# Optimization experiments

Measured on AMD Instinct MI355X. Metric: run time of the kernel, lower is better.

Reference implementation:

```python
import jax, jax.numpy as jnp
import numpy as np
import math

D_EMB = 1024
N_HEADS = 16
D_HEAD = D_EMB // N_HEADS
D_FF = 4 * D_EMB
BATCH = 2
SEQ = 2048
EPS = 1e-6


def setup_inputs() -> dict:
    key = jax.random.key(0)
    ks = jax.random.split(key, 12)
    s = 0.02
    return {
        "x": jax.random.normal(ks[0], (BATCH, SEQ, D_EMB), jnp.float32),
        "wq": jax.random.normal(ks[1], (D_EMB, D_EMB), jnp.float32) * s,
        "wk": jax.random.normal(ks[2], (D_EMB, D_EMB), jnp.float32) * s,
        "wv": jax.random.normal(ks[3], (D_EMB, D_EMB), jnp.float32) * s,
        "wo": jax.random.normal(ks[4], (D_EMB, D_EMB), jnp.float32) * s,
        "bo": jnp.zeros((D_EMB,), jnp.float32),
        "w1": jax.random.normal(ks[5], (D_FF, D_EMB), jnp.float32) * s,
        "b1": jnp.zeros((D_FF,), jnp.float32),
        "w2": jax.random.normal(ks[6], (D_EMB, D_FF), jnp.float32) * s,
        "b2": jnp.zeros((D_EMB,), jnp.float32),
        "ln1_s": jnp.ones((D_EMB,), jnp.float32),
        "ln1_b": jnp.zeros((D_EMB,), jnp.float32),
        "ln2_s": jnp.ones((D_EMB,), jnp.float32),
        "ln2_b": jnp.zeros((D_EMB,), jnp.float32),
    }


def _layernorm(x, scale, shift):
    mean = jnp.mean(x, axis=-1, keepdims=True)
    var = jnp.mean(jnp.square(x - mean), axis=-1, keepdims=True)  # unbiased=False
    return scale * (x - mean) / jnp.sqrt(var + EPS) + shift


def _gelu_tanh(x):
    c = math.sqrt(2.0 / math.pi)
    return 0.5 * x * (1.0 + jnp.tanh(c * (x + 0.044715 * x * x * x)))


def _attention(x, wq, wk, wv, wo, bo):
    B, S, _ = x.shape
    q = (x @ wq.T).reshape(B, S, N_HEADS, D_HEAD).transpose(0, 2, 1, 3)
    k = (x @ wk.T).reshape(B, S, N_HEADS, D_HEAD).transpose(0, 2, 1, 3)
    v = (x @ wv.T).reshape(B, S, N_HEADS, D_HEAD).transpose(0, 2, 1, 3)
    scores = jnp.einsum("bhqd,bhkd->bhqk", q, k)
    causal = jnp.triu(jnp.ones((S, S), bool), k=1)
    scores = jnp.where(causal, -jnp.inf, scores)
    weights = jax.nn.softmax(scores / math.sqrt(D_HEAD), axis=-1)
    ctx = jnp.einsum("bhqk,bhkd->bhqd", weights, v)
    ctx = ctx.transpose(0, 2, 1, 3).reshape(B, S, D_EMB)
    return ctx @ wo.T + bo


def reference(x, wq, wk, wv, wo, bo, w1, b1, w2, b2, ln1_s, ln1_b, ln2_s, ln2_b):
    # pre-norm attention block (dropout in eval mode = identity)
    h = x + _attention(_layernorm(x, ln1_s, ln1_b), wq, wk, wv, wo, bo)
    # pre-norm MLP with tanh-approx GeLU
    y = _layernorm(h, ln2_s, ln2_b)
    y = _gelu_tanh(y @ w1.T + b1) @ w2.T + b2
    return h + y
```

## Files before the change

kernel.cpp:

```cpp
#include <hip/hip_runtime.h>
#include <math.h>

typedef unsigned short u16;
typedef __attribute__((ext_vector_type(8))) __bf16 bf16x8v;
typedef __attribute__((ext_vector_type(8))) unsigned short ushort8v;
typedef __attribute__((ext_vector_type(4))) unsigned short ushort4v;
typedef __attribute__((ext_vector_type(4))) float f32x4v;

#define D_EMBD 1024
#define NHEADS 16
#define DHEAD  64
#define DFF    4096
#define BATCHN 2
#define SEQL   2048
#define TOK    (BATCHN*SEQL)

#define EPI_BF16_GELU    2
#define EPI_BF16_QKV     3
#define EPI_BF16_PART    5

__device__ __forceinline__ float bf2f(u16 s) {
  return __builtin_bit_cast(float, (unsigned)s << 16);
}
__device__ __forceinline__ u16 f2bf(float f) {
  unsigned u = __builtin_bit_cast(unsigned, f);
  unsigned r = u + 0x7fffu + ((u >> 16) & 1u);
  return (u16)(r >> 16);
}
__device__ __forceinline__ u16 f2bf_trunc(float f) {
  return (u16)(__builtin_bit_cast(unsigned, f) >> 16);
}

#define GLOAD16(gp, lp)                                                        \
  __builtin_amdgcn_global_load_lds(                                            \
      (__attribute__((address_space(1))) void*)(void*)(gp),                    \
      (__attribute__((address_space(3))) void*)(void*)(lp), 16, 0, 0)

__global__ __launch_bounds__(256) void cvt_all_kernel(const float* __restrict__ wq,
                                                      const float* __restrict__ wk,
                                                      const float* __restrict__ wv,
                                                      const float* __restrict__ wo,
                                                      const float* __restrict__ w1,
                                                      const float* __restrict__ w2,
                                                      u16* __restrict__ wcat,
                                                      u16* __restrict__ wob,
                                                      u16* __restrict__ w1b,
                                                      u16* __restrict__ w2b) {
  int bid = blockIdx.x;
  const float* src;
  u16* dst;
  int loc;
  if (bid < 4096) {
    int seg = bid >> 10;
    loc = (bid & 1023) * 256 + threadIdx.x;
    src = (seg == 0) ? wq : (seg == 1) ? wk : (seg == 2) ? wv : wo;
    dst = (seg == 0) ? wcat : (seg == 1) ? wcat + 1048576
                            : (seg == 2) ? wcat + 2097152 : wob;
  } else if (bid < 8192) {
    loc = (bid - 4096) * 256 + threadIdx.x;
    src = w1; dst = w1b;
  } else {
    loc = (bid - 8192) * 256 + threadIdx.x;
    src = w2; dst = w2b;
  }
  float4 v = ((const float4*)src)[loc];
  ushort4 o;
  o.x = f2bf(v.x); o.y = f2bf(v.y); o.z = f2bf(v.z); o.w = f2bf(v.w);
  ((ushort4*)dst)[loc] = o;
}

__global__ __launch_bounds__(256) void ln_kernel(const float* __restrict__ x,
                                                 const float* __restrict__ sc,
                                                 const float* __restrict__ sh,
                                                 u16* __restrict__ out) {
  int row = blockIdx.x, tid = threadIdx.x;
  const float4* xr = (const float4*)(x + (size_t)row * D_EMBD);
  float4 v = xr[tid];
  float s  = (v.x + v.y) + (v.z + v.w);
  float s2 = (v.x * v.x + v.y * v.y) + (v.z * v.z + v.w * v.w);
#pragma unroll
  for (int off = 32; off; off >>= 1) {
    s  += __shfl_xor(s, off, 64);
    s2 += __shfl_xor(s2, off, 64);
  }
  __shared__ float rs[4], rs2[4];
  int wave = tid >> 6, lane = tid & 63;
  if (lane == 0) { rs[wave] = s; rs2[wave] = s2; }
  __syncthreads();
  s  = (rs[0] + rs[1]) + (rs[2] + rs[3]);
  s2 = (rs2[0] + rs2[1]) + (rs2[2] + rs2[3]);
  float mean = s * (1.f / 1024.f);
  float var  = s2 * (1.f / 1024.f) - mean * mean;
  float rstd = rsqrtf(var + 1e-6f);
  float4 scv = ((const float4*)sc)[tid];
  float4 shv = ((const float4*)sh)[tid];
  ushort4 o;
  o.x = f2bf((v.x - mean) * rstd * scv.x + shv.x);
  o.y = f2bf((v.y - mean) * rstd * scv.y + shv.y);
  o.z = f2bf((v.z - mean) * rstd * scv.z + shv.z);
  o.w = f2bf((v.w - mean) * rstd * scv.w + shv.w);
  ((ushort4*)(out + (size_t)row * D_EMBD))[tid] = o;
}

__global__ __launch_bounds__(256) void ln2f_kernel(const u16* __restrict__ parts,
                                                   const float* __restrict__ x,
                                                   const float* __restrict__ bo,
                                                   const float* __restrict__ sc,
                                                   const float* __restrict__ sh,
                                                   float* __restrict__ hbuf,
                                                   u16* __restrict__ ybuf) {
  int row = blockIdx.x, tid = threadIdx.x;
  size_t base4 = (size_t)row * 256 + tid;
  float4 v = ((const float4*)x)[base4];
  float4 bv = ((const float4*)bo)[tid];
  v.x += bv.x; v.y += bv.y; v.z += bv.z; v.w += bv.w;
#pragma unroll
  for (int p = 0; p < 4; ++p) {
    ushort4 u = ((const ushort4*)parts)[(size_t)p * 1048576 + base4];
    v.x += bf2f(u.x); v.y += bf2f(u.y); v.z += bf2f(u.z); v.w += bf2f(u.w);
  }
  ((float4*)hbuf)[base4] = v;
  float s  = (v.x + v.y) + (v.z + v.w);
  float s2 = (v.x * v.x + v.y * v.y) + (v.z * v.z + v.w * v.w);
#pragma unroll
  for (int off = 32; off; off >>= 1) {
    s  += __shfl_xor(s, off, 64);
    s2 += __shfl_xor(s2, off, 64);
  }
  __shared__ float rs[4], rs2[4];
  int wave = tid >> 6, lane = tid & 63;
  if (lane == 0) { rs[wave] = s; rs2[wave] = s2; }
  __syncthreads();
  s  = (rs[0] + rs[1]) + (rs[2] + rs[3]);
  s2 = (rs2[0] + rs2[1]) + (rs2[2] + rs2[3]);
  float mean = s * (1.f / 1024.f);
  float var  = s2 * (1.f / 1024.f) - mean * mean;
  float rstd = rsqrtf(var + 1e-6f);
  float4 scv = ((const float4*)sc)[tid];
  float4 shv = ((const float4*)sh)[tid];
  ushort4 o;
  o.x = f2bf((v.x - mean) * rstd * scv.x + shv.x);
  o.y = f2bf((v.y - mean) * rstd * scv.y + shv.y);
  o.z = f2bf((v.z - mean) * rstd * scv.z + shv.z);
  o.w = f2bf((v.w - mean) * rstd * scv.w + shv.w);
  ((ushort4*)ybuf)[base4] = o;
}

__global__ __launch_bounds__(256) void reduce_w2_kernel(const u16* __restrict__ parts,
                                                        const float* __restrict__ resid,
                                                        const float* __restrict__ bias,
                                                        float* __restrict__ out) {
  int i = blockIdx.x * 256 + threadIdx.x;
  float4 r = ((const float4*)resid)[i];
  float4 bi = ((const float4*)bias)[i & 255];
  float s0 = 0, s1 = 0, s2 = 0, s3 = 0;
#pragma unroll
  for (int p = 0; p < 4; ++p) {
    ushort4 u = ((const ushort4*)parts)[(size_t)p * 1048576 + i];
    s0 += bf2f(u.x); s1 += bf2f(u.y); s2 += bf2f(u.z); s3 += bf2f(u.w);
  }
  float4 o = {s0 + r.x + bi.x, s1 + r.y + bi.y, s2 + r.z + bi.z, s3 + r.w + bi.w};
  ((float4*)out)[i] = o;
}

#define GBAR  __builtin_amdgcn_s_barrier()
#define LGKM0 do { asm volatile("s_waitcnt lgkmcnt(0)" ::: "memory"); \
                   __builtin_amdgcn_sched_barrier(0); } while (0)

template <int EPI>
__global__ __launch_bounds__(512, 2) void gemm256(const u16* __restrict__ A,
                                                  const u16* __restrict__ W,
                                                  u16* __restrict__ Cb,
                                                  const float* __restrict__ bias,
                                                  int M, int N, int K) {
  __shared__ __align__(16) u16 sm[65536];
  const int tid = threadIdx.x;
  const int wave = tid >> 6, lane = tid & 63;
  const int lr = lane & 15, quad = lane >> 4;
  const int wm = wave >> 2, wn = wave & 3;
  const int gx = gridDim.x, gy = gridDim.y;
  const int nwg = gx * gy * gridDim.z;
  const int bid = blockIdx.x + gx * (blockIdx.y + gy * blockIdx.z);
  const int swz = (bid & 7) * (nwg >> 3) + (bid >> 3);
  const int bx = swz % gx;
  const int r1 = swz / gx;
  const int by = r1 % gy, bz = r1 / gy;
  const int m0 = by * 256, n0 = bx * 256;
  const int KC = K / gridDim.z;
  const int kbeg = bz * KC;
  const int NT = KC >> 6;
  const size_t poff = (size_t)bz * ((size_t)M * N);

  const int r8 = lane >> 3;
  const int sslot = (lane & 7) ^ r8;
  const int rb0 = wave * 2;
  const int sx = lr & 7;

  auto stA = [&](int bb, int h, int tk) {
#pragma unroll
    for (int s = 0; s < 2; ++s) {
      const u16* gp = A + (size_t)(m0 + h * 128 + (rb0 + s) * 8 + r8) * K +
                      (kbeg + tk * 64 + sslot * 8);
      GLOAD16(gp, (char*)sm + bb * 65536 + h * 16384 + (rb0 + s) * 1024);
    }
  };
  auto stB = [&](int bb, int h, int tk) {
#pragma unroll
    for (int s = 0; s < 2; ++s) {
      const u16* gp = W + (size_t)(n0 + h * 128 + (rb0 + s) * 8 + r8) * K +
                      (kbeg + tk * 64 + sslot * 8);
      GLOAD16(gp, (char*)sm + bb * 65536 + 32768 + h * 16384 + (rb0 + s) * 1024);
    }
  };
  auto ldA = [&](bf16x8v (&av)[4][2], int mh, int cur) {
#pragma unroll
    for (int j2 = 0; j2 < 4; ++j2) {
      int row = (2 * (mh * 4 + j2) + wm) * 16 + lr;
#pragma unroll
      for (int kk = 0; kk < 2; ++kk) {
        int slot = (kk * 4 + quad) ^ sx;
        av[j2][kk] = *(const bf16x8v*)(sm + cur * 32768 + row * 64 + slot * 8);
      }
    }
  };
  auto ldB = [&](bf16x8v (&bv)[2][2], int nh, int cur) {
#pragma unroll
    for (int i2 = 0; i2 < 2; ++i2) {
      int row = (wn + 4 * (nh * 2 + i2)) * 16 + lr;
#pragma unroll
      for (int kk = 0; kk < 2; ++kk) {
        int slot = (kk * 4 + quad) ^ sx;
        bv[i2][kk] = *(const bf16x8v*)(sm + cur * 32768 + 16384 + row * 64 + slot * 8);
      }
    }
  };

  f32x4v acc[8][4];
#pragma unroll
  for (int j = 0; j < 8; ++j)
#pragma unroll
    for (int i = 0; i < 4; ++i) {
      f32x4v z = {0.f, 0.f, 0.f, 0.f};
      acc[j][i] = z;
    }
  bf16x8v av[4][2], bv0[2][2], bv1[2][2];

  auto MMA = [&](int mh, int nh, bf16x8v (&a)[4][2], bf16x8v (&b)[2][2]) {
    GBAR;
    LGKM0;
    __builtin_amdgcn_s_setprio(1);
#pragma unroll
    for (int j2 = 0; j2 < 4; ++j2)
#pragma unroll
      for (int i2 = 0; i2 < 2; ++i2)
#pragma unroll
        for (int kk = 0; kk < 2; ++kk)
          acc[mh * 4 + j2][nh * 2 + i2] = __builtin_amdgcn_mfma_f32_16x16x32_bf16(
              a[j2][kk], b[i2][kk], acc[mh * 4 + j2][nh * 2 + i2], 0, 0, 0);
    __builtin_amdgcn_s_setprio(0);
    __builtin_amdgcn_sched_barrier(0);
    GBAR;
  };

  stA(0, 0, 0); stB(0, 0, 0); stA(0, 1, 0); stB(0, 1, 0);
  stA(1, 0, 1); stB(1, 1, 1);
  asm volatile("s_waitcnt vmcnt(4)" ::: "memory");
  GBAR;

  for (int t = 0; t < NT; ++t) {
    const int cur = t & 1, nb = cur ^ 1;
    const bool p1 = (t + 1 < NT), p2 = (t + 2 < NT);
    ldA(av, 0, cur); ldB(bv0, 0, cur);
    if (p1) stB(nb, 0, t + 1);
    MMA(0, 0, av, bv0);
    ldB(bv1, 1, cur);
    if (p1) stA(nb, 1, t + 1);
    MMA(0, 1, av, bv1);
    ldA(av, 1, cur);
    if (p2) stA(cur, 0, t + 2);
    MMA(1, 1, av, bv1);
    if (p2) stB(cur, 1, t + 2);
    if (p2) { asm volatile("s_waitcnt vmcnt(4)" ::: "memory"); }
    else    { asm volatile("s_waitcnt vmcnt(0)" ::: "memory"); }
    MMA(1, 0, av, bv0);
  }

  const bool qsc = (EPI == EPI_BF16_QKV) && (n0 < 1024);
#pragma unroll
  for (int j = 0; j < 8; ++j) {
    int gr = m0 + (2 * j + wm) * 16 + quad * 4;
#pragma unroll
    for (int i = 0; i < 4; ++i) {
      int gc = n0 + (wn + 4 * i) * 16 + lr;
      float bi = 0.f;
      if constexpr (EPI == EPI_BF16_GELU) bi = bias[gc];
#pragma unroll
      for (int r = 0; r < 4; ++r) {
        size_t idx = (size_t)(gr + r) * N + gc;
        float v = acc[j][i][r];
        if constexpr (EPI == EPI_BF16_PART) {
          Cb[poff + idx] = f2bf(v);
        } else if constexpr (EPI == EPI_BF16_QKV) {
          Cb[idx] = f2bf(qsc ? v * 0.125f : v);
        } else {
          v += bi;
          float z = 0.7978845608028654f * (v + 0.044715f * v * v * v);
          float tt = 2.f / (1.f + __expf(-2.f * z)) - 1.f;
          Cb[idx] = f2bf(0.5f * v * (1.f + tt));
        }
      }
    }
  }
}

#define VTS 72
__device__ __forceinline__ void stage_k8(const u16* Kbase, int ks, u16* kfbuf,
                                         int wave, int lr, int quad) {
  int key = ((wave >> 1) << 4) + lr;
  int c8 = ((wave & 1) << 2) + quad;
  GLOAD16(Kbase + (size_t)(ks + key) * 3072 + c8 * 8, (char*)kfbuf + wave * 1024);
}
__device__ __forceinline__ void load_v(const u16* Vbase, int ks, int vkey0, int vc8,
                                       ushort8v& va, ushort8v& vb) {
  va = *(const ushort8v*)(Vbase + (size_t)(ks + vkey0) * 3072 + vc8 * 8);
  vb = *(const ushort8v*)(Vbase + (size_t)(ks + vkey0 + 1) * 3072 + vc8 * 8);
}
__device__ __forceinline__ void write_vt(u16* vt, int vc8, int vcol,
                                         ushort8v va, ushort8v vb) {
#pragma unroll
  for (int j = 0; j < 8; ++j) {
    unsigned pk = (unsigned)va[j] | ((unsigned)vb[j] << 16);
    *(unsigned*)(vt + (size_t)(vc8 * 8 + j) * VTS + vcol) = pk;
  }
}

__global__ __launch_bounds__(512) void attn_kernel(const u16* __restrict__ qkv,
                                                   u16* __restrict__ ctx) {
  __shared__ u16 Kf[2][4096];
  __shared__ u16 Vt[2][64 * VTS];
  int tid = threadIdx.x;
  int wave = tid >> 6, lane = tid & 63;
  int lr = lane & 15, quad = lane >> 4;
  int id = blockIdx.x;
  int bh = id & 31;
  int t = 15 - (id >> 5);
  int b = bh >> 4, h = bh & 15;
  int q0 = t * 128;
  const u16* qkvb = qkv + (size_t)(b * SEQL) * 3072;
  int qrow = q0 + wave * 16 + lr;
  const u16* Qp = qkvb + (size_t)qrow * 3072 + h * 64 + quad * 8;
  bf16x8v qf0 = *(const bf16x8v*)(Qp);
  bf16x8v qf1 = *(const bf16x8v*)(Qp + 32);
  const u16* Kbase = qkvb + 1024 + h * 64;
  const u16* Vbase = qkvb + 2048 + h * 64;
  const bool vstager = (tid < 256);
  int vkey0 = ((tid & 255) >> 3) * 2, vc8 = tid & 7;
  int vcol = vkey0 ^ (vc8 << 2);

  float m = -INFINITY, l = 0.f;
  f32x4v accO[4];
#pragma unroll
  for (int r = 0; r < 4; r++) {
    f32x4v z = {0.f, 0.f, 0.f, 0.f};
    accO[r] = z;
  }

  int nkt = 2 * t + 2;
  {
    stage_k8(Kbase, 0, Kf[0], wave, lr, quad);
    if (vstager) {
      ushort8v va, vb;
      load_v(Vbase, 0, vkey0, vc8, va, vb);
      write_vt(Vt[0], vc8, vcol, va, vb);
    }
  }
  __syncthreads();

  for (int kt = 0; kt < nkt; ++kt) {
    int cur = kt & 1, nxt = cur ^ 1;
    ushort8v va, vb;
    bool pre = (kt + 1 < nkt);
    if (pre) {
      stage_k8(Kbase, (kt + 1) * 64, Kf[nxt], wave, lr, quad);
      if (vstager) load_v(Vbase, (kt + 1) * 64, vkey0, vc8, va, vb);
    }
    bool active = !(kt == 2 * t + 1 && wave < 4);
    if (active) {
      const bf16x8v* Kc = (const bf16x8v*)Kf[cur];
      const u16* Vc = Vt[cur];
      f32x4v accS[4];
#pragma unroll
      for (int jb = 0; jb < 4; jb++) {
        f32x4v z = {0.f, 0.f, 0.f, 0.f};
        accS[jb] = z;
      }
#pragma unroll
      for (int jb = 0; jb < 4; jb++) {
        accS[jb] = __builtin_amdgcn_mfma_f32_16x16x32_bf16(Kc[((jb * 2 + 0) << 6) + lane], qf0, accS[jb], 0, 0, 0);
        accS[jb] = __builtin_amdgcn_mfma_f32_16x16x32_bf16(Kc[((jb * 2 + 1) << 6) + lane], qf1, accS[jb], 0, 0, 0);
      }
      if (kt >= 2 * t) {
        int kb = (kt - 2 * t) << 6;
#pragma unroll
        for (int jb = 0; jb < 4; jb++)
#pragma unroll
          for (int r = 0; r < 4; r++)
            if (kb + jb * 16 + quad * 4 + r > wave * 16 + lr) accS[jb][r] = -INFINITY;
      }
      float smax = accS[0][0];
#pragma unroll
      for (int jb = 0; jb < 4; jb++)
#pragma unroll
        for (int r = 0; r < 4; r++) smax = fmaxf(smax, accS[jb][r]);
      smax = fmaxf(smax, __shfl_xor(smax, 16, 64));
      smax = fmaxf(smax, __shfl_xor(smax, 32, 64));
      float mn = fmaxf(m, smax);
      float alpha = __expf(m - mn);
      m = mn;
      float ps = 0.f;
#pragma unroll
      for (int jb = 0; jb < 4; jb++)
#pragma unroll
        for (int r = 0; r < 4; r++) {
          accS[jb][r] = __expf(accS[jb][r] - mn);
          ps += accS[jb][r];
        }
      ps += __shfl_xor(ps, 16, 64);
      ps += __shfl_xor(ps, 32, 64);
      l = l * alpha + ps;
      float ar[4];
#pragma unroll
      for (int r = 0; r < 4; r++) ar[r] = __shfl(alpha, quad * 4 + r, 16);
#pragma unroll
      for (int nb = 0; nb < 4; nb++)
#pragma unroll
        for (int r = 0; r < 4; r++) accO[nb][r] *= ar[r];
#pragma unroll
      for (int kk = 0; kk < 2; ++kk) {
        ushort8v pp;
#pragma unroll
        for (int j = 0; j < 4; ++j) {
          pp[j]     = f2bf_trunc(accS[2 * kk][j]);
          pp[j + 4] = f2bf_trunc(accS[2 * kk + 1][j]);
        }
        bf16x8v pav = __builtin_bit_cast(bf16x8v, pp);
#pragma unroll
        for (int nb = 0; nb < 4; nb++) {
          int dim = nb * 16 + lr;
          int f = (nb * 2 + (lr >> 3)) & 7;
          int col1 = (kk * 32 + quad * 4) ^ (f << 2);
          ushort4v v0 = *(const ushort4v*)(Vc + dim * VTS + col1);
          ushort4v v1 = *(const ushort4v*)(Vc + dim * VTS + (col1 ^ 16));
          ushort8v vv;
#pragma unroll
          for (int j = 0; j < 4; ++j) { vv[j] = v0[j]; vv[j + 4] = v1[j]; }
          accO[nb] = __builtin_amdgcn_mfma_f32_16x16x32_bf16(pav, __builtin_bit_cast(bf16x8v, vv), accO[nb], 0, 0, 0);
        }
      }
    }
    if (pre && vstager) write_vt(Vt[nxt], vc8, vcol, va, vb);
    __syncthreads();
  }
  float linv = 1.f / l;
  float rr[4];
#pragma unroll
  for (int r = 0; r < 4; r++) rr[r] = __shfl(linv, quad * 4 + r, 16);
#pragma unroll
  for (int nb = 0; nb < 4; nb++)
#pragma unroll
    for (int r = 0; r < 4; r++) {
      int rowg = q0 + wave * 16 + quad * 4 + r;
      ctx[(size_t)(b * SEQL + rowg) * D_EMBD + h * 64 + nb * 16 + lr] =
          f2bf(accO[nb][r] * rr[r]);
    }
}

extern "C" void kernel_launch(void* const* d_in, const int* in_sizes, int n_in,
                              void* d_out, int out_size, void* d_ws, size_t ws_size,
                              hipStream_t stream) {
  const float* x    = (const float*)d_in[0];
  const float* wq   = (const float*)d_in[1];
  const float* wk   = (const float*)d_in[2];
  const float* wv   = (const float*)d_in[3];
  const float* wo   = (const float*)d_in[4];
  const float* bo   = (const float*)d_in[5];
  const float* w1   = (const float*)d_in[6];
  const float* b1   = (const float*)d_in[7];
  const float* w2   = (const float*)d_in[8];
  const float* b2   = (const float*)d_in[9];
  const float* ln1s = (const float*)d_in[10];
  const float* ln1b = (const float*)d_in[11];
  const float* ln2s = (const float*)d_in[12];
  const float* ln2b = (const float*)d_in[13];
  float* out = (float*)d_out;

  char* base = (char*)d_ws;
  size_t off = 0;
  auto alloc = [&](size_t bytes) {
    char* r = base + off;
    off += (bytes + 255) & ~(size_t)255;
    return r;
  };
  u16*   wcat = (u16*)alloc((size_t)3072 * 1024 * 2);
  u16*   wob  = (u16*)alloc((size_t)1024 * 1024 * 2);
  u16*   w1b  = (u16*)alloc((size_t)4096 * 1024 * 2);
  u16*   w2b  = (u16*)alloc((size_t)1024 * 4096 * 2);
  u16*   xn   = (u16*)alloc((size_t)TOK * 1024 * 2);
  u16*   qkv  = (u16*)alloc((size_t)TOK * 3072 * 2);
  u16*   ctx  = (u16*)alloc((size_t)TOK * 1024 * 2);
  float* hbuf = (float*)alloc((size_t)TOK * 1024 * 4);
  u16*   ybuf = (u16*)alloc((size_t)TOK * 1024 * 2);
  u16*   gbuf = (u16*)alloc((size_t)TOK * 4096 * 2);
  u16* woP = (u16*)xn;
  u16* w2P = (u16*)xn;

  cvt_all_kernel<<<12288, 256, 0, stream>>>(wq, wk, wv, wo, w1, w2,
                                            wcat, wob, w1b, w2b);
  ln_kernel<<<TOK, 256, 0, stream>>>(x, ln1s, ln1b, xn);
  gemm256<EPI_BF16_QKV><<<dim3(12, 16), 512, 0, stream>>>(
      xn, wcat, qkv, nullptr, TOK, 3072, 1024);
  attn_kernel<<<512, 512, 0, stream>>>(qkv, ctx);
  gemm256<EPI_BF16_PART><<<dim3(4, 16, 4), 512, 0, stream>>>(
      ctx, wob, woP, nullptr, TOK, 1024, 1024);
  ln2f_kernel<<<TOK, 256, 0, stream>>>(woP, x, bo, ln2s, ln2b, hbuf, ybuf);
  gemm256<EPI_BF16_GELU><<<dim3(16, 16), 512, 0, stream>>>(
      ybuf, w1b, gbuf, b1, TOK, 4096, 1024);
  gemm256<EPI_BF16_PART><<<dim3(4, 16, 4), 512, 0, stream>>>(
      gbuf, w2b, w2P, nullptr, TOK, 1024, 4096);
  reduce_w2_kernel<<<4096, 256, 0, stream>>>(w2P, hbuf, b2, out);
}
```

Measured before the change: 334.6 us.

## Triple-buffer K tiles in attention and use partial vmcnt waits

Attention now keeps three K tiles in LDS and issues the async global-to-LDS K load two iterations ahead. The per-iteration __syncthreads is replaced by explicit lgkmcnt/vmcnt waits plus s_barrier, so the newest K load can stay in flight across the barrier. This is meant to hide global load latency behind the MFMA work. It costs extra LDS, which may lower occupancy, and correctness depends on the hand-counted vmcnt matching the outstanding loads.

```diff
diff --git a/kernel.cpp b/kernel.cpp
--- a/kernel.cpp
+++ b/kernel.cpp
@@ -336,7 +336,7 @@
 
 __global__ __launch_bounds__(512) void attn_kernel(const u16* __restrict__ qkv,
                                                    u16* __restrict__ ctx) {
-  __shared__ u16 Kf[2][4096];
+  __shared__ u16 Kf[3][4096];
   __shared__ u16 Vt[2][64 * VTS];
   int tid = threadIdx.x;
   int wave = tid >> 6, lane = tid & 63;
@@ -367,27 +367,27 @@
 
   int nkt = 2 * t + 2;
   {
+    ushort8v va, vb;
+    if (vstager) load_v(Vbase, 0, vkey0, vc8, va, vb);
     stage_k8(Kbase, 0, Kf[0], wave, lr, quad);
-    if (vstager) {
-      ushort8v va, vb;
-      load_v(Vbase, 0, vkey0, vc8, va, vb);
-      write_vt(Vt[0], vc8, vcol, va, vb);
-    }
-  }
-  __syncthreads();
-
+    stage_k8(Kbase, 64, Kf[1], wave, lr, quad);
+    if (vstager) write_vt(Vt[0], vc8, vcol, va, vb);
+    asm volatile("s_waitcnt lgkmcnt(0)" ::: "memory");
+    asm volatile("s_waitcnt vmcnt(1)" ::: "memory");
+    __builtin_amdgcn_s_barrier();
+    __builtin_amdgcn_sched_barrier(0);
+  }
+
+  int k0 = 0, k1 = 1, k2 = 2;
   for (int kt = 0; kt < nkt; ++kt) {
-    int cur = kt & 1, nxt = cur ^ 1;
     ushort8v va, vb;
-    bool pre = (kt + 1 < nkt);
-    if (pre) {
-      stage_k8(Kbase, (kt + 1) * 64, Kf[nxt], wave, lr, quad);
-      if (vstager) load_v(Vbase, (kt + 1) * 64, vkey0, vc8, va, vb);
-    }
-    bool active = !(kt == 2 * t + 1 && wave < 4);
+    bool pre = (kt + 1 < nkt), pre2 = (kt + 2 < nkt);
+    if (pre && vstager) load_v(Vbase, (kt + 1) * 64, vkey0, vc8, va, vb);
+    if (pre2) stage_k8(Kbase, (kt + 2) * 64, Kf[k2], wave, lr, quad);
+    bool active = !(kt == nkt - 1 && wave < 4);
     if (active) {
-      const bf16x8v* Kc = (const bf16x8v*)Kf[cur];
-      const u16* Vc = Vt[cur];
+      const bf16x8v* Kc = (const bf16x8v*)Kf[k0];
+      const u16* Vc = Vt[kt & 1];
       f32x4v accS[4];
 #pragma unroll
       for (int jb = 0; jb < 4; jb++) {
@@ -458,8 +458,15 @@
         }
       }
     }
-    if (pre && vstager) write_vt(Vt[nxt], vc8, vcol, va, vb);
-    __syncthreads();
+    if (pre && vstager) write_vt(Vt[(kt + 1) & 1], vc8, vcol, va, vb);
+    if (pre) {
+      asm volatile("s_waitcnt lgkmcnt(0)" ::: "memory");
+      if (pre2) { asm volatile("s_waitcnt vmcnt(1)" ::: "memory"); }
+      else      { asm volatile("s_waitcnt vmcnt(0)" ::: "memory"); }
+      __builtin_amdgcn_s_barrier();
+      __builtin_amdgcn_sched_barrier(0);
+    }
+    int tmpk = k0; k0 = k1; k1 = k2; k2 = tmpk;
   }
   float linv = 1.f / l;
   float rr[4];
```

Measured after the change: 336.9 us. No clear change (+0.7%).
